# Kernel optimization log

Measured on AMD Instinct MI355X. Metric: run time of the kernel, lower is better.

The kernel has to match this reference:

```python
import jax, jax.numpy as jnp
import numpy as np

NEG_SLOPE = 0.2

def gat_layer(x, src, dst, W, a_src, a_dst, b):
    # PyG GATConv (concat=True, self-loops already appended to src/dst)
    N = x.shape[0]
    H, C = a_src.shape
    h = (x @ W).reshape(N, H, C)                      # [N,H,C]
    alpha_s = jnp.einsum('nhc,hc->nh', h, a_src)      # [N,H]
    alpha_d = jnp.einsum('nhc,hc->nh', h, a_dst)
    e = jax.nn.leaky_relu(alpha_s[src] + alpha_d[dst], NEG_SLOPE)  # [E,H]
    # scatter-softmax over edges grouped by destination node
    m = jax.ops.segment_max(e, dst, num_segments=N)
    e = jnp.exp(e - m[dst])
    denom = jax.ops.segment_sum(e, dst, num_segments=N)
    alpha = e / (denom[dst] + 1e-16)                  # [E,H]
    msg = h[src] * alpha[:, :, None]                  # [E,H,C]
    out = jax.ops.segment_sum(msg, dst, num_segments=N)
    return out.reshape(N, H * C) + b


def setup_inputs() -> dict:
    key = jax.random.key(0)
    ks = jax.random.split(key, 16)
    N, E, B = 20000, 640000, 32
    in_f, out_dim = 128, 512
    x = jax.random.normal(ks[0], (N, in_f), dtype=jnp.float32)
    edge_index = jax.random.randint(ks[1], (2, E), 0, N, dtype=jnp.int64)
    batch = jnp.sort(jax.random.randint(ks[2], (N,), 0, B, dtype=jnp.int64))
    def p(k, shape):
        return jax.random.normal(k, shape, dtype=jnp.float32) * 0.1
    inp = {
        'x': x, 'edge_index': edge_index, 'batch': batch,
        'W1': p(ks[3], (in_f, 256)), 'a1_src': p(ks[4], (4, 64)), 'a1_dst': p(ks[5], (4, 64)), 'b1': jnp.zeros((256,), jnp.float32),
        'W2': p(ks[6], (256, 256)), 'a2_src': p(ks[7], (4, 64)), 'a2_dst': p(ks[8], (4, 64)), 'b2': jnp.zeros((256,), jnp.float32),
        'W3': p(ks[9], (256, 256)), 'a3_src': p(ks[10], (4, 64)), 'a3_dst': p(ks[11], (4, 64)), 'b3': jnp.zeros((256,), jnp.float32),
        'W4': p(ks[12], (256, 512)), 'a4_src': p(ks[13], (4, 128)), 'a4_dst': p(ks[14], (4, 128)), 'b4': jnp.zeros((512,), jnp.float32),
        'fcW': p(ks[15], (1024, out_dim)), 'fcb': jnp.zeros((out_dim,), jnp.float32),
    }
    return inp


def reference(x, edge_index, batch, W1, a1_src, a1_dst, b1, W2, a2_src, a2_dst, b2,
              W3, a3_src, a3_dst, b3, W4, a4_src, a4_dst, b4, fcW, fcb):
    N = x.shape[0]
    B = 32
    loops = jnp.arange(N, dtype=edge_index.dtype)
    src = jnp.concatenate([edge_index[0], loops])
    dst = jnp.concatenate([edge_index[1], loops])
    h = jax.nn.elu(gat_layer(x, src, dst, W1, a1_src, a1_dst, b1))
    h = jax.nn.elu(gat_layer(h, src, dst, W2, a2_src, a2_dst, b2))
    h = jax.nn.elu(gat_layer(h, src, dst, W3, a3_src, a3_dst, b3))
    h = jax.nn.elu(gat_layer(h, src, dst, W4, a4_src, a4_dst, b4))   # [N,512]
    cnt = jax.ops.segment_sum(jnp.ones((N,), h.dtype), batch, num_segments=B)
    x_mean = jax.ops.segment_sum(h, batch, num_segments=B) / jnp.maximum(cnt, 1.0)[:, None]
    x_max = jax.ops.segment_max(h, batch, num_segments=B)
    x_max = jnp.where(jnp.isfinite(x_max), x_max, 0.0)
    g = jnp.concatenate([x_mean, x_max], axis=1)                     # [B,1024]
    return g @ fcW + fcb
```

## Files before the change

### kernel.cpp

```cpp
#include <hip/hip_runtime.h>
#include <math.h>

#define WAVE 64

typedef __attribute__((ext_vector_type(4))) float f32x4;
typedef _Float16 h16x4 __attribute__((ext_vector_type(4)));
typedef _Float16 h16x8 __attribute__((ext_vector_type(8)));

__device__ __forceinline__ float selh(float e0, float e1, float e2, float e3, int m){
  float r = (m == 1) ? e1 : e0;
  r = (m == 2) ? e2 : r;
  r = (m == 3) ? e3 : r;
  return r;
}

__global__ void k_zero_i(int* p, int n){
  int i = blockIdx.x*blockDim.x + threadIdx.x;
  if (i < n) p[i] = 0;
}

__global__ void k_count(const int* __restrict__ ei, int E, int N, int* __restrict__ cnt){
  int i = blockIdx.x*blockDim.x + threadIdx.x;
  if (i >= E + N) return;
  int d = (i < E) ? ei[E + i] : (i - E);
  atomicAdd(&cnt[d], 1);
}

__global__ __launch_bounds__(1024)
void k_scan1(const int* __restrict__ cnt, int* __restrict__ rp, int* __restrict__ bsum, int N){
  __shared__ int sd[1024];
  int t = threadIdx.x, i = blockIdx.x*1024 + t;
  int v = (i < N) ? cnt[i] : 0;
  sd[t] = v;
  __syncthreads();
  for (int off = 1; off < 1024; off <<= 1){
    int x = (t >= off) ? sd[t-off] : 0;
    __syncthreads();
    sd[t] += x;
    __syncthreads();
  }
  if (i < N) rp[i] = sd[t] - v;
  if (t == 1023) bsum[blockIdx.x] = sd[1023];
}

__global__ void k_scan2(int* __restrict__ bsum, int nb, int* __restrict__ rp, int N){
  int t = threadIdx.x;
  int orig = (t < nb) ? bsum[t] : 0;
  int v = orig;
  #pragma unroll
  for (int off = 1; off < 64; off <<= 1){
    int x = __shfl_up(v, off, WAVE);
    if (t >= off) v += x;
  }
  if (t < nb) bsum[t] = v - orig;
  if (t == 63) rp[N] = v;
}

__global__ __launch_bounds__(1024)
void k_scan3(int* __restrict__ rp, int* __restrict__ cur, const int* __restrict__ bsum, int N){
  int i = blockIdx.x*1024 + threadIdx.x;
  if (i < N){
    int v = rp[i] + bsum[blockIdx.x];
    rp[i] = v;
    cur[i] = v;
  }
}

__global__ void k_fill(const int* __restrict__ ei, int E, int N,
                       int* __restrict__ cur, int* __restrict__ es){
  int i = blockIdx.x*blockDim.x + threadIdx.x;
  if (i >= E + N) return;
  int s, d;
  if (i < E){ s = ei[i]; d = ei[E + i]; } else { s = d = i - E; }
  int pos = atomicAdd(&cur[d], 1);
  es[pos] = s;
}

__global__ void k_bounds(const int* __restrict__ batch, int N, int B, int* __restrict__ bs){
  int b = blockIdx.x*blockDim.x + threadIdx.x;
  if (b > B) return;
  int lo = 0, hi = N;
  while (lo < hi){ int mid = (lo + hi) >> 1; if (batch[mid] < b) lo = mid + 1; else hi = mid; }
  bs[b] = lo;
}

__global__ __launch_bounds__(256)
void k_cvt16(const float* __restrict__ in, _Float16* __restrict__ out, int n4){
  int i = blockIdx.x*blockDim.x + threadIdx.x;
  if (i >= n4) return;
  float4 v = ((const float4*)in)[i];
  h16x4 o;
  o[0] = (_Float16)v.x; o[1] = (_Float16)v.y;
  o[2] = (_Float16)v.z; o[3] = (_Float16)v.w;
  ((h16x4*)out)[i] = o;
}

__global__ __launch_bounds__(256)
void k_cvt_w_all(const float* __restrict__ W0, const float* __restrict__ W1,
                 const float* __restrict__ W2, const float* __restrict__ W3,
                 _Float16* __restrict__ out){
  int i = blockIdx.x*blockDim.x + threadIdx.x;
  if (i < 32768){
    int k = i >> 8, n = i & 255;
    out[(size_t)n*128 + k] = (_Float16)W0[i];
  } else if (i < 98304){
    int j = i - 32768;
    int k = j >> 8, n = j & 255;
    out[32768 + (size_t)n*256 + k] = (_Float16)W1[j];
  } else if (i < 163840){
    int j = i - 98304;
    int k = j >> 8, n = j & 255;
    out[98304 + (size_t)n*256 + k] = (_Float16)W2[j];
  } else if (i < 294912){
    int j = i - 163840;
    int k = j >> 9, n = j & 511;
    out[163840 + (size_t)n*256 + k] = (_Float16)W3[j];
  }
}

template<int CHEAD>
__global__ __launch_bounds__(512)
void k_gemm_fused(const _Float16* __restrict__ Ax, const _Float16* __restrict__ Bw,
                  _Float16* __restrict__ Ch,
                  const float* __restrict__ asr, const float* __restrict__ adt,
                  float* __restrict__ as4, float* __restrict__ ad4,
                  int M, int K, int Nc){
  constexpr int LDP = 40;
  __shared__ _Float16 sA[2][128*LDP], sB[2][128*LDP];
  const int tid = threadIdx.x;
  const int m0 = blockIdx.x*128, n0 = blockIdx.y*128;
  const int w = tid >> 6, l = tid & 63;
  const int wr = w >> 1, wc = w & 1;
  const int sr = tid >> 2, sc = (tid & 3)*8;

  f32x4 acc00={0.f,0.f,0.f,0.f}, acc01=acc00, acc02=acc00, acc03=acc00;
  f32x4 acc10=acc00, acc11=acc00, acc12=acc00, acc13=acc00;

  const int arow = m0 + sr;
  const bool aval = arow < M;
  const size_t aoff = (size_t)arow*K + sc;
  const size_t boff = (size_t)(n0 + sr)*K + sc;

  const int fa0 = (wr*32 + (l & 15))*LDP + (l >> 4)*8;
  const int fa1 = fa0 + 16*LDP;
  const int fb0 = (wc*64 + (l & 15))*LDP + (l >> 4)*8;
  const int steps = K >> 5;

  uint4 va = make_uint4(0,0,0,0), vb;
  if (aval) va = *(const uint4*)(Ax + aoff);
  vb = *(const uint4*)(Bw + boff);
  *(uint4*)&sA[0][sr*LDP + sc] = va;
  *(uint4*)&sB[0][sr*LDP + sc] = vb;
  __syncthreads();

  for (int ks = 0; ks < steps; ++ks){
    const int cur = ks & 1;
    const bool more = (ks + 1 < steps);
    if (more){
      const int k0 = (ks + 1)*32;
      va = make_uint4(0,0,0,0);
      if (aval) va = *(const uint4*)(Ax + aoff + k0);
      vb = *(const uint4*)(Bw + boff + k0);
    }

    h16x8 a0 = *(const h16x8*)&sA[cur][fa0];
    h16x8 a1 = *(const h16x8*)&sA[cur][fa1];
    h16x8 b;
    b = *(const h16x8*)&sB[cur][fb0];
    acc00 = __builtin_amdgcn_mfma_f32_16x16x32_f16(a0, b, acc00, 0, 0, 0);
    acc10 = __builtin_amdgcn_mfma_f32_16x16x32_f16(a1, b, acc10, 0, 0, 0);
    b = *(const h16x8*)&sB[cur][fb0 + 16*LDP];
    acc01 = __builtin_amdgcn_mfma_f32_16x16x32_f16(a0, b, acc01, 0, 0, 0);
    acc11 = __builtin_amdgcn_mfma_f32_16x16x32_f16(a1, b, acc11, 0, 0, 0);
    b = *(const h16x8*)&sB[cur][fb0 + 32*LDP];
    acc02 = __builtin_amdgcn_mfma_f32_16x16x32_f16(a0, b, acc02, 0, 0, 0);
    acc12 = __builtin_amdgcn_mfma_f32_16x16x32_f16(a1, b, acc12, 0, 0, 0);
    b = *(const h16x8*)&sB[cur][fb0 + 48*LDP];
    acc03 = __builtin_amdgcn_mfma_f32_16x16x32_f16(a0, b, acc03, 0, 0, 0);
    acc13 = __builtin_amdgcn_mfma_f32_16x16x32_f16(a1, b, acc13, 0, 0, 0);

    if (more){
      *(uint4*)&sA[cur^1][sr*LDP + sc] = va;
      *(uint4*)&sB[cur^1][sr*LDP + sc] = vb;
      __syncthreads();
    }
  }

  const int colb = n0 + wc*64 + (l & 15);
  const float ca0 = asr[colb], ca1 = asr[colb+16], ca2 = asr[colb+32], ca3 = asr[colb+48];
  const float cd0 = adt[colb], cd1 = adt[colb+16], cd2 = adt[colb+32], cd3 = adt[colb+48];

  float psA[1]; (void)psA;

  float psm0[4], pdm0[4], psm1[4], pdm1[4];
  {
    const int rb = m0 + wr*32 + (l >> 4)*4;
    #pragma unroll
    for (int j = 0; j < 4; ++j){
      int row = rb + j;
      if (row < M){
        _Float16* hp = Ch + (size_t)row*Nc + colb;
        hp[0]  = (_Float16)acc00[j];
        hp[16] = (_Float16)acc01[j];
        hp[32] = (_Float16)acc02[j];
        hp[48] = (_Float16)acc03[j];
      }
      float ps = ca0*acc00[j] + ca1*acc01[j] + ca2*acc02[j] + ca3*acc03[j];
      float pd = cd0*acc00[j] + cd1*acc01[j] + cd2*acc02[j] + cd3*acc03[j];
      ps += __shfl_xor(ps, 1, WAVE);  pd += __shfl_xor(pd, 1, WAVE);
      ps += __shfl_xor(ps, 2, WAVE);  pd += __shfl_xor(pd, 2, WAVE);
      ps += __shfl_xor(ps, 4, WAVE);  pd += __shfl_xor(pd, 4, WAVE);
      ps += __shfl_xor(ps, 8, WAVE);  pd += __shfl_xor(pd, 8, WAVE);
      psm0[j] = ps; pdm0[j] = pd;
    }
  }
  {
    const int rb = m0 + wr*32 + 16 + (l >> 4)*4;
    #pragma unroll
    for (int j = 0; j < 4; ++j){
      int row = rb + j;
      if (row < M){
        _Float16* hp = Ch + (size_t)row*Nc + colb;
        hp[0]  = (_Float16)acc10[j];
        hp[16] = (_Float16)acc11[j];
        hp[32] = (_Float16)acc12[j];
        hp[48] = (_Float16)acc13[j];
      }
      float ps = ca0*acc10[j] + ca1*acc11[j] + ca2*acc12[j] + ca3*acc13[j];
      float pd = cd0*acc10[j] + cd1*acc11[j] + cd2*acc12[j] + cd3*acc13[j];
      ps += __shfl_xor(ps, 1, WAVE);  pd += __shfl_xor(pd, 1, WAVE);
      ps += __shfl_xor(ps, 2, WAVE);  pd += __shfl_xor(pd, 2, WAVE);
      ps += __shfl_xor(ps, 4, WAVE);  pd += __shfl_xor(pd, 4, WAVE);
      ps += __shfl_xor(ps, 8, WAVE);  pd += __shfl_xor(pd, 8, WAVE);
      psm1[j] = ps; pdm1[j] = pd;
    }
  }

  if (CHEAD == 64){
    const int hy = blockIdx.y*2 + wc;
    if ((l & 15) == 0){
      const int rb0 = m0 + wr*32 + (l >> 4)*4;
      #pragma unroll
      for (int j = 0; j < 4; ++j){
        int row = rb0 + j;
        if (row < M){ as4[(size_t)row*4 + hy] = psm0[j]; ad4[(size_t)row*4 + hy] = pdm0[j]; }
      }
      const int rb1 = rb0 + 16;
      #pragma unroll
      for (int j = 0; j < 4; ++j){
        int row = rb1 + j;
        if (row < M){ as4[(size_t)row*4 + hy] = psm1[j]; ad4[(size_t)row*4 + hy] = pdm1[j]; }
      }
    }
  } else {
    float* red = (float*)&sA[0][0];
    __syncthreads();
    if ((l & 15) == 0){
      const int lr0 = wr*32 + (l >> 4)*4;
      #pragma unroll
      for (int j = 0; j < 4; ++j){
        red[(lr0 + j)*4 + wc*2 + 0] = psm0[j];
        red[(lr0 + j)*4 + wc*2 + 1] = pdm0[j];
      }
      const int lr1 = lr0 + 16;
      #pragma unroll
      for (int j = 0; j < 4; ++j){
        red[(lr1 + j)*4 + wc*2 + 0] = psm1[j];
        red[(lr1 + j)*4 + wc*2 + 1] = pdm1[j];
      }
    }
    __syncthreads();
    if (tid < 128){
      int row = m0 + tid;
      if (row < M){
        float ps = red[tid*4 + 0] + red[tid*4 + 2];
        float pd = red[tid*4 + 1] + red[tid*4 + 3];
        as4[(size_t)row*4 + blockIdx.y] = ps;
        ad4[(size_t)row*4 + blockIdx.y] = pd;
      }
    }
  }
}

template<int HC, int WF32>
__global__ __launch_bounds__(256)
void k_agg_h(const int* __restrict__ rp, const int* __restrict__ es,
             const float* __restrict__ as4, const float* __restrict__ ad4,
             const _Float16* __restrict__ h, const float* __restrict__ bias,
             float* __restrict__ outF, _Float16* __restrict__ oH, int N){
  constexpr int VEC = HC / 64;
  int wid  = (blockIdx.x*blockDim.x + threadIdx.x) >> 6;
  int lane = threadIdx.x & 63;
  if (wid >= N) return;
  int beg = rp[wid], end = rp[wid+1];

  const float4 adv = *(const float4*)(ad4 + (size_t)wid*4);
  const float ad0 = adv.x, ad1 = adv.y, ad2 = adv.z, ad3 = adv.w;

  float m0=-1e30f, m1=-1e30f, m2=-1e30f, m3=-1e30f;
  float s0=0.f, s1=0.f, s2=0.f, s3=0.f;
  for (int i = beg + lane; i < end; i += WAVE){
    int s = es[i];
    const float4 av = *(const float4*)(as4 + (size_t)s*4);
    float e, mn;
    e = av.x + ad0; e = (e >= 0.f) ? e : 0.2f*e;
    mn = fmaxf(m0, e); s0 = s0*__expf(m0-mn) + __expf(e-mn); m0 = mn;
    e = av.y + ad1; e = (e >= 0.f) ? e : 0.2f*e;
    mn = fmaxf(m1, e); s1 = s1*__expf(m1-mn) + __expf(e-mn); m1 = mn;
    e = av.z + ad2; e = (e >= 0.f) ? e : 0.2f*e;
    mn = fmaxf(m2, e); s2 = s2*__expf(m2-mn) + __expf(e-mn); m2 = mn;
    e = av.w + ad3; e = (e >= 0.f) ? e : 0.2f*e;
    mn = fmaxf(m3, e); s3 = s3*__expf(m3-mn) + __expf(e-mn); m3 = mn;
  }
  #pragma unroll
  for (int off = 32; off > 0; off >>= 1){
    float mo, so, mn;
    mo = __shfl_xor(m0, off, WAVE); so = __shfl_xor(s0, off, WAVE);
    mn = fmaxf(m0, mo); s0 = s0*__expf(m0-mn) + so*__expf(mo-mn); m0 = mn;
    mo = __shfl_xor(m1, off, WAVE); so = __shfl_xor(s1, off, WAVE);
    mn = fmaxf(m1, mo); s1 = s1*__expf(m1-mn) + so*__expf(mo-mn); m1 = mn;
    mo = __shfl_xor(m2, off, WAVE); so = __shfl_xor(s2, off, WAVE);
    mn = fmaxf(m2, mo); s2 = s2*__expf(m2-mn) + so*__expf(mo-mn); m2 = mn;
    mo = __shfl_xor(m3, off, WAVE); so = __shfl_xor(s3, off, WAVE);
    mn = fmaxf(m3, mo); s3 = s3*__expf(m3-mn) + so*__expf(mo-mn); m3 = mn;
  }
  const float i0 = 1.f/(s0 + 1e-16f), i1 = 1.f/(s1 + 1e-16f);
  const float i2 = 1.f/(s2 + 1e-16f), i3 = 1.f/(s3 + 1e-16f);
  const int myh = lane >> 4;

  float ac[VEC] = {};

  for (int cb = beg; cb < end; cb += WAVE){
    int nn = min(WAVE, end - cb);
    int sidx = 0;
    float w0 = 0.f, w1 = 0.f, w2 = 0.f, w3 = 0.f;
    if (cb + lane < end){
      sidx = es[cb + lane];
      const float4 av = *(const float4*)(as4 + (size_t)sidx*4);
      float e;
      e = av.x + ad0; e = (e >= 0.f) ? e : 0.2f*e; w0 = __expf(e - m0)*i0;
      e = av.y + ad1; e = (e >= 0.f) ? e : 0.2f*e; w1 = __expf(e - m1)*i1;
      e = av.z + ad2; e = (e >= 0.f) ? e : 0.2f*e; w2 = __expf(e - m2)*i2;
      e = av.w + ad3; e = (e >= 0.f) ? e : 0.2f*e; w3 = __expf(e - m3)*i3;
    }

    int j = 0;
    for (; j + 4 <= nn; j += 4){
      int sj0 = __shfl(sidx, j+0, WAVE), sj1 = __shfl(sidx, j+1, WAVE);
      int sj2 = __shfl(sidx, j+2, WAVE), sj3 = __shfl(sidx, j+3, WAVE);
      float u0 = selh(__shfl(w0,j+0,WAVE), __shfl(w1,j+0,WAVE), __shfl(w2,j+0,WAVE), __shfl(w3,j+0,WAVE), myh);
      float u1 = selh(__shfl(w0,j+1,WAVE), __shfl(w1,j+1,WAVE), __shfl(w2,j+1,WAVE), __shfl(w3,j+1,WAVE), myh);
      float u2 = selh(__shfl(w0,j+2,WAVE), __shfl(w1,j+2,WAVE), __shfl(w2,j+2,WAVE), __shfl(w3,j+2,WAVE), myh);
      float u3 = selh(__shfl(w0,j+3,WAVE), __shfl(w1,j+3,WAVE), __shfl(w2,j+3,WAVE), __shfl(w3,j+3,WAVE), myh);
      if (VEC == 4){
        h16x4 v0 = *(const h16x4*)(h + (size_t)sj0*HC + lane*4);
        h16x4 v1 = *(const h16x4*)(h + (size_t)sj1*HC + lane*4);
        h16x4 v2 = *(const h16x4*)(h + (size_t)sj2*HC + lane*4);
        h16x4 v3 = *(const h16x4*)(h + (size_t)sj3*HC + lane*4);
        #pragma unroll
        for (int c = 0; c < 4; ++c)
          ac[c] = fmaf(u0,(float)v0[c], fmaf(u1,(float)v1[c], fmaf(u2,(float)v2[c], fmaf(u3,(float)v3[c], ac[c]))));
      } else {
        h16x8 v0 = *(const h16x8*)(h + (size_t)sj0*HC + lane*8);
        h16x8 v1 = *(const h16x8*)(h + (size_t)sj1*HC + lane*8);
        h16x8 v2 = *(const h16x8*)(h + (size_t)sj2*HC + lane*8);
        h16x8 v3 = *(const h16x8*)(h + (size_t)sj3*HC + lane*8);
        #pragma unroll
        for (int c = 0; c < VEC; ++c)
          ac[c] = fmaf(u0,(float)v0[c], fmaf(u1,(float)v1[c], fmaf(u2,(float)v2[c], fmaf(u3,(float)v3[c], ac[c]))));
      }
    }
    for (; j < nn; ++j){
      int sj = __shfl(sidx, j, WAVE);
      float u = selh(__shfl(w0,j,WAVE), __shfl(w1,j,WAVE), __shfl(w2,j,WAVE), __shfl(w3,j,WAVE), myh);
      if (VEC == 4){
        h16x4 v = *(const h16x4*)(h + (size_t)sj*HC + lane*4);
        #pragma unroll
        for (int c = 0; c < 4; ++c) ac[c] = fmaf(u, (float)v[c], ac[c]);
      } else {
        h16x8 v = *(const h16x8*)(h + (size_t)sj*HC + lane*8);
        #pragma unroll
        for (int c = 0; c < VEC; ++c) ac[c] = fmaf(u, (float)v[c], ac[c]);
      }
    }
  }

  float r0=0,r1=0,r2=0,r3=0,r4=0,r5=0,r6=0,r7=0;
  {
    const float* bp = bias + lane*VEC;
    #pragma unroll
    for (int c = 0; c < VEC; ++c){
      float r = ac[c] + bp[c];
      r = r > 0.f ? r : expm1f(r);
      if (c==0) r0=r; else if (c==1) r1=r; else if (c==2) r2=r; else if (c==3) r3=r;
      else if (c==4) r4=r; else if (c==5) r5=r; else if (c==6) r6=r; else r7=r;
    }
  }
  if (WF32){
    float* op = outF + (size_t)wid*HC + lane*VEC;
    *(float4*)op = make_float4(r0,r1,r2,r3);
    if (VEC == 8) *(float4*)(op+4) = make_float4(r4,r5,r6,r7);
  } else {
    h16x4 o;
    o[0] = (_Float16)r0; o[1] = (_Float16)r1;
    o[2] = (_Float16)r2; o[3] = (_Float16)r3;
    *(h16x4*)(oH + (size_t)wid*HC + lane*VEC) = o;
    if (VEC == 8){
      h16x4 o2;
      o2[0] = (_Float16)r4; o2[1] = (_Float16)r5;
      o2[2] = (_Float16)r6; o2[3] = (_Float16)r7;
      *(h16x4*)(oH + (size_t)wid*HC + lane*VEC + 4) = o2;
    }
  }
}

__global__ void k_pool_partial(const float* __restrict__ h, const int* __restrict__ bs,
                               float* __restrict__ psum, float* __restrict__ pmax){
  int b = blockIdx.x, ch = blockIdx.y;
  int f = threadIdx.x;
  int s = bs[b], e = bs[b+1];
  long long len = e - s;
  int i0 = s + (int)(len * ch / 8);
  int i1 = s + (int)(len * (ch+1) / 8);
  float sm = 0.f, mx = -3.0e38f;
  for (int i = i0; i < i1; ++i){
    float v = h[(size_t)i*512 + f];
    sm += v; mx = fmaxf(mx, v);
  }
  int idx = (b*8 + ch)*512 + f;
  psum[idx] = sm; pmax[idx] = mx;
}

__global__ void k_pool_final(const float* __restrict__ psum, const float* __restrict__ pmax,
                             const int* __restrict__ bs, float* __restrict__ g){
  int b = blockIdx.x, f = threadIdx.x;
  float sm = 0.f, mx = -3.0e38f;
  for (int c = 0; c < 8; ++c){
    int idx = (b*8 + c)*512 + f;
    sm += psum[idx]; mx = fmaxf(mx, pmax[idx]);
  }
  int cnt = bs[b+1] - bs[b];
  g[b*1024 + f] = sm / fmaxf((float)cnt, 1.f);
  g[b*1024 + 512 + f] = (mx > -1e37f) ? mx : 0.f;
}

__global__ __launch_bounds__(256)
void k_fc(const float* __restrict__ g, const float* __restrict__ fcW,
          const float* __restrict__ fcb, float* __restrict__ out){
  __shared__ float gs[1024];
  __shared__ float red[4][64];
  int b = blockIdx.x, t = threadIdx.x;
  int o0 = blockIdx.y * 64;
  for (int i = t; i < 1024; i += 256) gs[i] = g[b*1024 + i];
  __syncthreads();
  int ol = t & 63, q = t >> 6;
  const float* wp = fcW + (size_t)(q*256)*512 + o0 + ol;
  float acc = 0.f;
  #pragma unroll 8
  for (int k = 0; k < 256; ++k)
    acc = fmaf(gs[q*256 + k], wp[(size_t)k*512], acc);
  red[q][ol] = acc;
  __syncthreads();
  if (t < 64){
    float r = red[0][t] + red[1][t] + red[2][t] + red[3][t] + fcb[o0 + t];
    out[b*512 + o0 + t] = r;
  }
}

extern "C" void kernel_launch(void* const* d_in, const int* in_sizes, int n_in,
                              void* d_out, int out_size, void* d_ws, size_t ws_size,
                              hipStream_t stream){
  (void)n_in; (void)out_size; (void)ws_size;
  const float* x     = (const float*)d_in[0];
  const int*   ei    = (const int*)d_in[1];
  const int*   batch = (const int*)d_in[2];
  const float* W[4]   = {(const float*)d_in[3],(const float*)d_in[7],(const float*)d_in[11],(const float*)d_in[15]};
  const float* asr[4] = {(const float*)d_in[4],(const float*)d_in[8],(const float*)d_in[12],(const float*)d_in[16]};
  const float* adt[4] = {(const float*)d_in[5],(const float*)d_in[9],(const float*)d_in[13],(const float*)d_in[17]};
  const float* bb[4]  = {(const float*)d_in[6],(const float*)d_in[10],(const float*)d_in[14],(const float*)d_in[18]};
  const float* fcW = (const float*)d_in[19];
  const float* fcb = (const float*)d_in[20];

  const int N  = in_sizes[0] / 128;
  const int E  = in_sizes[1] / 2;
  const int EN = E + N;
  const int B  = 32;
  const int NB = (N + 1023) / 1024;

  char* p = (char*)d_ws;
  auto alloc = [&](size_t bytes){ void* r = (void*)p; p += (bytes + 255) & ~(size_t)255; return r; };
  float* bufA = (float*)alloc((size_t)N*512*4);
  _Float16* hA = (_Float16*)alloc((size_t)N*512*2);
  _Float16* hB = (_Float16*)alloc((size_t)N*512*2);
  _Float16* Wh = (_Float16*)alloc((size_t)294912*2);
  float* a2   = (float*)alloc((size_t)N*8*4);
  float* as4 = a2;
  float* ad4 = a2 + (size_t)N*4;
  int*   cnt  = (int*)alloc((size_t)N*4);
  int*   rp   = (int*)alloc((size_t)(N+1)*4);
  int*   cur  = (int*)alloc((size_t)N*4);
  int*   es   = (int*)alloc((size_t)EN*4);
  int*   bs   = (int*)alloc((size_t)(B+1)*4);
  int*   bsum = (int*)alloc((size_t)64*4);
  float* gpo  = (float*)alloc((size_t)B*1024*4);
  float* psum = (float*)alloc((size_t)B*8*512*4);
  float* pmax = (float*)alloc((size_t)B*8*512*4);

  k_zero_i<<<(N+255)/256, 256, 0, stream>>>(cnt, N);
  k_count<<<(EN+255)/256, 256, 0, stream>>>(ei, E, N, cnt);
  k_scan1<<<NB, 1024, 0, stream>>>(cnt, rp, bsum, N);
  k_scan2<<<1, 64, 0, stream>>>(bsum, NB, rp, N);
  k_scan3<<<NB, 1024, 0, stream>>>(rp, cur, bsum, N);
  k_fill<<<(EN+255)/256, 256, 0, stream>>>(ei, E, N, cur, es);
  k_bounds<<<1, 64, 0, stream>>>(batch, N, B, bs);

  k_cvt16<<<((N*128/4) + 255)/256, 256, 0, stream>>>(x, hB, N*128/4);
  k_cvt_w_all<<<(294912 + 255)/256, 256, 0, stream>>>(W[0], W[1], W[2], W[3], Wh);

  const int wgrid = (N + 3) / 4;
  const int Kd[4]  = {128, 256, 256, 256};
  const int HCd[4] = {256, 256, 256, 512};
  const size_t Woff[4] = {0, 32768, 98304, 163840};

  for (int L = 0; L < 4; ++L){
    const int K = Kd[L], Nc = HCd[L];
    dim3 gg((N + 127)/128, Nc/128);
    if (Nc == 256)
      k_gemm_fused<64><<<gg, 512, 0, stream>>>(hB, Wh + Woff[L], hA, asr[L], adt[L], as4, ad4, N, K, Nc);
    else
      k_gemm_fused<128><<<gg, 512, 0, stream>>>(hB, Wh + Woff[L], hA, asr[L], adt[L], as4, ad4, N, K, Nc);
    if (L < 3)
      k_agg_h<256,0><<<wgrid, 256, 0, stream>>>(rp, es, as4, ad4, hA, bb[L], (float*)nullptr, hB, N);
    else
      k_agg_h<512,1><<<wgrid, 256, 0, stream>>>(rp, es, as4, ad4, hA, bb[L], bufA, (_Float16*)nullptr, N);
  }

  dim3 pg(B, 8);
  k_pool_partial<<<pg, 512, 0, stream>>>(bufA, bs, psum, pmax);
  k_pool_final<<<B, 512, 0, stream>>>(psum, pmax, bs, gpo);
  dim3 fg(B, 8);
  k_fc<<<fg, 256, 0, stream>>>(gpo, fcW, fcb, (float*)d_out);
}
```

Before: 447.8 us.

## Merge preprocessing kernels, fold scan stages, store final layer in fp16

Fuses degree counting, input/weight fp16 conversion and batch-bound search into one multi-role launch, and replaces the zeroing kernel with a memset. The block-sum scan stage is folded into scan1 via a last-block-done atomic. The pool-final stage is merged into the fc kernel. The last aggregation layer now writes fp16 instead of fp32. The aim is fewer launches and less memory traffic, at the cost of fp16 rounding of the final features before pooling and a serial last-block scan.

```diff
diff --git a/kernel.cpp b/kernel.cpp
--- a/kernel.cpp
+++ b/kernel.cpp
@@ -14,20 +14,58 @@
   return r;
 }
 
-__global__ void k_zero_i(int* p, int n){
-  int i = blockIdx.x*blockDim.x + threadIdx.x;
-  if (i < n) p[i] = 0;
-}
-
-__global__ void k_count(const int* __restrict__ ei, int E, int N, int* __restrict__ cnt){
-  int i = blockIdx.x*blockDim.x + threadIdx.x;
-  if (i >= E + N) return;
-  int d = (i < E) ? ei[E + i] : (i - E);
-  atomicAdd(&cnt[d], 1);
+__global__ __launch_bounds__(256)
+void k_front(const int* __restrict__ ei, int E, int N, int* __restrict__ cnt,
+             const float* __restrict__ x, _Float16* __restrict__ hB,
+             const float* __restrict__ W0, const float* __restrict__ W1,
+             const float* __restrict__ W2, const float* __restrict__ W3,
+             _Float16* __restrict__ Wh,
+             const int* __restrict__ batch, int B, int* __restrict__ bs,
+             int CB, int XB, int WB){
+  int bid = blockIdx.x, t = threadIdx.x;
+  if (bid < CB){
+    int i = bid*256 + t;
+    if (i < E + N){
+      int d = (i < E) ? ei[E + i] : (i - E);
+      atomicAdd(&cnt[d], 1);
+    }
+  } else if (bid < CB + XB){
+    int i = (bid - CB)*256 + t;
+    if (i < N*32){
+      float4 v = ((const float4*)x)[i];
+      h16x4 o;
+      o[0] = (_Float16)v.x; o[1] = (_Float16)v.y;
+      o[2] = (_Float16)v.z; o[3] = (_Float16)v.w;
+      ((h16x4*)hB)[i] = o;
+    }
+  } else if (bid < CB + XB + WB){
+    int i = (bid - CB - XB)*256 + t;
+    if (i < 32768){
+      int k = i >> 8, n = i & 255;
+      Wh[(size_t)n*128 + k] = (_Float16)W0[i];
+    } else if (i < 98304){
+      int j = i - 32768; int k = j >> 8, n = j & 255;
+      Wh[32768 + (size_t)n*256 + k] = (_Float16)W1[j];
+    } else if (i < 163840){
+      int j = i - 98304; int k = j >> 8, n = j & 255;
+      Wh[98304 + (size_t)n*256 + k] = (_Float16)W2[j];
+    } else if (i < 294912){
+      int j = i - 163840; int k = j >> 9, n = j & 511;
+      Wh[163840 + (size_t)n*256 + k] = (_Float16)W3[j];
+    }
+  } else {
+    int b = t;
+    if (b <= B){
+      int lo = 0, hi = N;
+      while (lo < hi){ int mid = (lo + hi) >> 1; if (batch[mid] < b) lo = mid + 1; else hi = mid; }
+      bs[b] = lo;
+    }
+  }
 }
 
 __global__ __launch_bounds__(1024)
-void k_scan1(const int* __restrict__ cnt, int* __restrict__ rp, int* __restrict__ bsum, int N){
+void k_scan1(const int* __restrict__ cnt, int* __restrict__ rp, int* __restrict__ bsum,
+             int* __restrict__ done, int N, int nb){
   __shared__ int sd[1024];
   int t = threadIdx.x, i = blockIdx.x*1024 + t;
   int v = (i < N) ? cnt[i] : 0;
@@ -41,19 +79,15 @@
   }
   if (i < N) rp[i] = sd[t] - v;
   if (t == 1023) bsum[blockIdx.x] = sd[1023];
-}
-
-__global__ void k_scan2(int* __restrict__ bsum, int nb, int* __restrict__ rp, int N){
-  int t = threadIdx.x;
-  int orig = (t < nb) ? bsum[t] : 0;
-  int v = orig;
-  #pragma unroll
-  for (int off = 1; off < 64; off <<= 1){
-    int x = __shfl_up(v, off, WAVE);
-    if (t >= off) v += x;
-  }
-  if (t < nb) bsum[t] = v - orig;
-  if (t == 63) rp[N] = v;
+  __threadfence();
+  __syncthreads();
+  if (t == 0){
+    if (atomicAdd(done, 1) == nb - 1){
+      int run = 0;
+      for (int b2 = 0; b2 < nb; ++b2){ int s = bsum[b2]; bsum[b2] = run; run += s; }
+      rp[N] = run;
+    }
+  }
 }
 
 __global__ __launch_bounds__(1024)
@@ -74,48 +108,6 @@
   if (i < E){ s = ei[i]; d = ei[E + i]; } else { s = d = i - E; }
   int pos = atomicAdd(&cur[d], 1);
   es[pos] = s;
-}
-
-__global__ void k_bounds(const int* __restrict__ batch, int N, int B, int* __restrict__ bs){
-  int b = blockIdx.x*blockDim.x + threadIdx.x;
-  if (b > B) return;
-  int lo = 0, hi = N;
-  while (lo < hi){ int mid = (lo + hi) >> 1; if (batch[mid] < b) lo = mid + 1; else hi = mid; }
-  bs[b] = lo;
-}
-
-__global__ __launch_bounds__(256)
-void k_cvt16(const float* __restrict__ in, _Float16* __restrict__ out, int n4){
-  int i = blockIdx.x*blockDim.x + threadIdx.x;
-  if (i >= n4) return;
-  float4 v = ((const float4*)in)[i];
-  h16x4 o;
-  o[0] = (_Float16)v.x; o[1] = (_Float16)v.y;
-  o[2] = (_Float16)v.z; o[3] = (_Float16)v.w;
-  ((h16x4*)out)[i] = o;
-}
-
-__global__ __launch_bounds__(256)
-void k_cvt_w_all(const float* __restrict__ W0, const float* __restrict__ W1,
-                 const float* __restrict__ W2, const float* __restrict__ W3,
-                 _Float16* __restrict__ out){
-  int i = blockIdx.x*blockDim.x + threadIdx.x;
-  if (i < 32768){
-    int k = i >> 8, n = i & 255;
-    out[(size_t)n*128 + k] = (_Float16)W0[i];
-  } else if (i < 98304){
-    int j = i - 32768;
-    int k = j >> 8, n = j & 255;
-    out[32768 + (size_t)n*256 + k] = (_Float16)W1[j];
-  } else if (i < 163840){
-    int j = i - 98304;
-    int k = j >> 8, n = j & 255;
-    out[98304 + (size_t)n*256 + k] = (_Float16)W2[j];
-  } else if (i < 294912){
-    int j = i - 163840;
-    int k = j >> 9, n = j & 511;
-    out[163840 + (size_t)n*256 + k] = (_Float16)W3[j];
-  }
 }
 
 template<int CHEAD>
@@ -190,8 +182,6 @@
   const float ca0 = asr[colb], ca1 = asr[colb+16], ca2 = asr[colb+32], ca3 = asr[colb+48];
   const float cd0 = adt[colb], cd1 = adt[colb+16], cd2 = adt[colb+32], cd3 = adt[colb+48];
 
-  float psA[1]; (void)psA;
-
   float psm0[4], pdm0[4], psm1[4], pdm1[4];
   {
     const int rb = m0 + wr*32 + (l >> 4)*4;
@@ -282,12 +272,12 @@
   }
 }
 
-template<int HC, int WF32>
+template<int HC>
 __global__ __launch_bounds__(256)
 void k_agg_h(const int* __restrict__ rp, const int* __restrict__ es,
              const float* __restrict__ as4, const float* __restrict__ ad4,
              const _Float16* __restrict__ h, const float* __restrict__ bias,
-             float* __restrict__ outF, _Float16* __restrict__ oH, int N){
+             _Float16* __restrict__ oH, int N){
   constexpr int VEC = HC / 64;
   int wid  = (blockIdx.x*blockDim.x + threadIdx.x) >> 6;
   int lane = threadIdx.x & 63;
@@ -396,25 +386,19 @@
       else if (c==4) r4=r; else if (c==5) r5=r; else if (c==6) r6=r; else r7=r;
     }
   }
-  if (WF32){
-    float* op = outF + (size_t)wid*HC + lane*VEC;
-    *(float4*)op = make_float4(r0,r1,r2,r3);
-    if (VEC == 8) *(float4*)(op+4) = make_float4(r4,r5,r6,r7);
-  } else {
-    h16x4 o;
-    o[0] = (_Float16)r0; o[1] = (_Float16)r1;
-    o[2] = (_Float16)r2; o[3] = (_Float16)r3;
-    *(h16x4*)(oH + (size_t)wid*HC + lane*VEC) = o;
-    if (VEC == 8){
-      h16x4 o2;
-      o2[0] = (_Float16)r4; o2[1] = (_Float16)r5;
-      o2[2] = (_Float16)r6; o2[3] = (_Float16)r7;
-      *(h16x4*)(oH + (size_t)wid*HC + lane*VEC + 4) = o2;
-    }
-  }
-}
-
-__global__ void k_pool_partial(const float* __restrict__ h, const int* __restrict__ bs,
+  h16x4 o;
+  o[0] = (_Float16)r0; o[1] = (_Float16)r1;
+  o[2] = (_Float16)r2; o[3] = (_Float16)r3;
+  *(h16x4*)(oH + (size_t)wid*HC + lane*VEC) = o;
+  if (VEC == 8){
+    h16x4 o2;
+    o2[0] = (_Float16)r4; o2[1] = (_Float16)r5;
+    o2[2] = (_Float16)r6; o2[3] = (_Float16)r7;
+    *(h16x4*)(oH + (size_t)wid*HC + lane*VEC + 4) = o2;
+  }
+}
+
+__global__ void k_pool_partial(const _Float16* __restrict__ h, const int* __restrict__ bs,
                                float* __restrict__ psum, float* __restrict__ pmax){
   int b = blockIdx.x, ch = blockIdx.y;
   int f = threadIdx.x;
@@ -424,34 +408,33 @@
   int i1 = s + (int)(len * (ch+1) / 8);
   float sm = 0.f, mx = -3.0e38f;
   for (int i = i0; i < i1; ++i){
-    float v = h[(size_t)i*512 + f];
+    float v = (float)h[(size_t)i*512 + f];
     sm += v; mx = fmaxf(mx, v);
   }
   int idx = (b*8 + ch)*512 + f;
   psum[idx] = sm; pmax[idx] = mx;
 }
 
-__global__ void k_pool_final(const float* __restrict__ psum, const float* __restrict__ pmax,
-                             const int* __restrict__ bs, float* __restrict__ g){
-  int b = blockIdx.x, f = threadIdx.x;
-  float sm = 0.f, mx = -3.0e38f;
-  for (int c = 0; c < 8; ++c){
-    int idx = (b*8 + c)*512 + f;
-    sm += psum[idx]; mx = fmaxf(mx, pmax[idx]);
-  }
-  int cnt = bs[b+1] - bs[b];
-  g[b*1024 + f] = sm / fmaxf((float)cnt, 1.f);
-  g[b*1024 + 512 + f] = (mx > -1e37f) ? mx : 0.f;
-}
-
 __global__ __launch_bounds__(256)
-void k_fc(const float* __restrict__ g, const float* __restrict__ fcW,
+void k_fc(const float* __restrict__ psum, const float* __restrict__ pmax,
+          const int* __restrict__ bs, const float* __restrict__ fcW,
           const float* __restrict__ fcb, float* __restrict__ out){
   __shared__ float gs[1024];
   __shared__ float red[4][64];
   int b = blockIdx.x, t = threadIdx.x;
   int o0 = blockIdx.y * 64;
-  for (int i = t; i < 1024; i += 256) gs[i] = g[b*1024 + i];
+  int cntb = bs[b+1] - bs[b];
+  float inv = 1.f / fmaxf((float)cntb, 1.f);
+  for (int i = t; i < 512; i += 256){
+    float sm = 0.f, mx = -3.0e38f;
+    #pragma unroll
+    for (int c = 0; c < 8; ++c){
+      int idx = (b*8 + c)*512 + i;
+      sm += psum[idx]; mx = fmaxf(mx, pmax[idx]);
+    }
+    gs[i] = sm * inv;
+    gs[512 + i] = (mx > -1e37f) ? mx : 0.f;
+  }
   __syncthreads();
   int ol = t & 63, q = t >> 6;
   const float* wp = fcW + (size_t)(q*256)*512 + o0 + ol;
@@ -489,33 +472,35 @@
 
   char* p = (char*)d_ws;
   auto alloc = [&](size_t bytes){ void* r = (void*)p; p += (bytes + 255) & ~(size_t)255; return r; };
-  float* bufA = (float*)alloc((size_t)N*512*4);
   _Float16* hA = (_Float16*)alloc((size_t)N*512*2);
   _Float16* hB = (_Float16*)alloc((size_t)N*512*2);
   _Float16* Wh = (_Float16*)alloc((size_t)294912*2);
   float* a2   = (float*)alloc((size_t)N*8*4);
   float* as4 = a2;
   float* ad4 = a2 + (size_t)N*4;
-  int*   cnt  = (int*)alloc((size_t)N*4);
+  int*   cntdone = (int*)alloc((size_t)(N+64)*4);
+  int*   cnt  = cntdone;
+  int*   done = cntdone + N;
   int*   rp   = (int*)alloc((size_t)(N+1)*4);
   int*   cur  = (int*)alloc((size_t)N*4);
   int*   es   = (int*)alloc((size_t)EN*4);
   int*   bs   = (int*)alloc((size_t)(B+1)*4);
   int*   bsum = (int*)alloc((size_t)64*4);
-  float* gpo  = (float*)alloc((size_t)B*1024*4);
   float* psum = (float*)alloc((size_t)B*8*512*4);
   float* pmax = (float*)alloc((size_t)B*8*512*4);
 
-  k_zero_i<<<(N+255)/256, 256, 0, stream>>>(cnt, N);
-  k_count<<<(EN+255)/256, 256, 0, stream>>>(ei, E, N, cnt);
-  k_scan1<<<NB, 1024, 0, stream>>>(cnt, rp, bsum, N);
-  k_scan2<<<1, 64, 0, stream>>>(bsum, NB, rp, N);
+  hipMemsetAsync(cntdone, 0, (size_t)(N+1)*4, stream);
+
+  const int CB = (EN + 255)/256;
+  const int XB = (N*32 + 255)/256;
+  const int WB = (294912 + 255)/256;
+  k_front<<<CB + XB + WB + 1, 256, 0, stream>>>(ei, E, N, cnt, x, hB,
+                                                W[0], W[1], W[2], W[3], Wh,
+                                                batch, B, bs, CB, XB, WB);
+
+  k_scan1<<<NB, 1024, 0, stream>>>(cnt, rp, bsum, done, N, NB);
   k_scan3<<<NB, 1024, 0, stream>>>(rp, cur, bsum, N);
   k_fill<<<(EN+255)/256, 256, 0, stream>>>(ei, E, N, cur, es);
-  k_bounds<<<1, 64, 0, stream>>>(batch, N, B, bs);
-
-  k_cvt16<<<((N*128/4) + 255)/256, 256, 0, stream>>>(x, hB, N*128/4);
-  k_cvt_w_all<<<(294912 + 255)/256, 256, 0, stream>>>(W[0], W[1], W[2], W[3], Wh);
 
   const int wgrid = (N + 3) / 4;
   const int Kd[4]  = {128, 256, 256, 256};
@@ -529,15 +514,14 @@
       k_gemm_fused<64><<<gg, 512, 0, stream>>>(hB, Wh + Woff[L], hA, asr[L], adt[L], as4, ad4, N, K, Nc);
     else
       k_gemm_fused<128><<<gg, 512, 0, stream>>>(hB, Wh + Woff[L], hA, asr[L], adt[L], as4, ad4, N, K, Nc);
-    if (L < 3)
-      k_agg_h<256,0><<<wgrid, 256, 0, stream>>>(rp, es, as4, ad4, hA, bb[L], (float*)nullptr, hB, N);
+    if (Nc == 256)
+      k_agg_h<256><<<wgrid, 256, 0, stream>>>(rp, es, as4, ad4, hA, bb[L], hB, N);
     else
-      k_agg_h<512,1><<<wgrid, 256, 0, stream>>>(rp, es, as4, ad4, hA, bb[L], bufA, (_Float16*)nullptr, N);
+      k_agg_h<512><<<wgrid, 256, 0, stream>>>(rp, es, as4, ad4, hA, bb[L], hB, N);
   }
 
   dim3 pg(B, 8);
-  k_pool_partial<<<pg, 512, 0, stream>>>(bufA, bs, psum, pmax);
-  k_pool_final<<<B, 512, 0, stream>>>(psum, pmax, bs, gpo);
+  k_pool_partial<<<pg, 512, 0, stream>>>(hB, bs, psum, pmax);
   dim3 fg(B, 8);
-  k_fc<<<fg, 256, 0, stream>>>(gpo, fcW, fcb, (float*)d_out);
-}
+  k_fc<<<fg, 256, 0, stream>>>(psum, pmax, bs, fcW, fcb, (float*)d_out);
+}
```

Result: no change. 440.8 us (-1.6%).
